# Optimization experiments

Measured on AMD Instinct MI355X. Metric: run time of the kernel, lower is better.

## Reference

```python
import jax, jax.numpy as jnp
import numpy as np

D_MODEL = 256
D_HID = 128
EPS = 1e-5
MASK_VALUE = -10000.0


def _layer_norm(x, scale, bias):
    mu = jnp.mean(x, axis=-1, keepdims=True)
    var = jnp.mean(jnp.square(x - mu), axis=-1, keepdims=True)
    return (x - mu) * jax.lax.rsqrt(var + EPS) * scale + bias


def setup_inputs() -> dict:
    key = jax.random.key(0)
    ks = jax.random.split(key, 8)
    B, S = 32, 1024
    std = 0.02
    return {
        "x": jax.random.normal(ks[0], (B, S, D_MODEL), dtype=jnp.float32),
        "ln1_scale": jnp.ones((D_MODEL,), jnp.float32),
        "ln1_bias": jnp.zeros((D_MODEL,), jnp.float32),
        "w_qkv": jax.random.normal(ks[1], (D_MODEL, 3 * D_MODEL), jnp.float32) * std,
        "b_qkv": jnp.zeros((3 * D_MODEL,), jnp.float32),
        "w_proj": jax.random.normal(ks[2], (D_MODEL, D_MODEL), jnp.float32) * std,
        "b_proj": jnp.zeros((D_MODEL,), jnp.float32),
        "ln2_scale": jnp.ones((D_MODEL,), jnp.float32),
        "ln2_bias": jnp.zeros((D_MODEL,), jnp.float32),
        "w_fc1": jax.random.normal(ks[3], (D_MODEL, D_HID), jnp.float32) * std,
        "b_fc1": jnp.zeros((D_HID,), jnp.float32),
        "w_fc2": jax.random.normal(ks[4], (D_HID, D_MODEL), jnp.float32) * std,
        "b_fc2": jnp.zeros((D_MODEL,), jnp.float32),
    }


def reference(x, ln1_scale, ln1_bias, w_qkv, b_qkv, w_proj, b_proj,
              ln2_scale, ln2_bias, w_fc1, b_fc1, w_fc2, b_fc2):
    B, S, D = x.shape
    # --- pre-LN self-attention ---
    residual = x
    h = _layer_norm(x, ln1_scale, ln1_bias)
    qkv = h @ w_qkv + b_qkv                       # [B, S, 3D]
    q, k, v = jnp.split(qkv, 3, axis=2)           # each [B, S, D]; 1 head, head_dim=D
    scale = 1.0 / jnp.sqrt(jnp.asarray(D, x.dtype))
    scores = jnp.einsum('bqd,bkd->bqk', q, k) * scale   # [B, S, S]
    causal = jnp.tril(jnp.ones((S, S), dtype=bool))
    scores = jnp.where(causal[None, :, :], scores, MASK_VALUE)
    attn = jax.nn.softmax(scores, axis=-1)        # dropout is identity (eval mode)
    out = jnp.einsum('bqk,bkd->bqd', attn, v)     # [B, S, D]
    out = out @ w_proj + b_proj
    x = out + residual
    # --- pre-LN MLP ---
    residual = x
    h = _layer_norm(x, ln2_scale, ln2_bias)
    h = jax.nn.relu(h @ w_fc1 + b_fc1)
    h = h @ w_fc2 + b_fc2
    return h + residual
```

## Files before the change

kernel.cpp:

```cpp
#include <hip/hip_runtime.h>
#include <hip/hip_bf16.h>

#define D_MODEL 256
#define D_HID   128
#define SEQ     1024
#define NBATCH  32
#define NROWS   (NBATCH * SEQ)
#define MASKV   -10000.0f
#define EPSLN   1e-5f

typedef unsigned short u16;
using bf16x8 = __attribute__((ext_vector_type(8))) short;
using f32x4  = __attribute__((ext_vector_type(4))) float;

union U8 { uint4 v; u16 s[8]; };

__device__ __forceinline__ float bf2f(u16 u) {
    unsigned int x = ((unsigned int)u) << 16;
    return __uint_as_float(x);
}
__device__ __forceinline__ u16 f2bf(float f) {
    unsigned int u = __float_as_uint(f);
    u += 0x7fff + ((u >> 16) & 1);
    return (u16)(u >> 16);
}
__device__ __forceinline__ void load4(const float* p, float* f) {
    float4 a = *(const float4*)p;
    f[0] = a.x; f[1] = a.y; f[2] = a.z; f[3] = a.w;
}
__device__ __forceinline__ void load4(const u16* p, float* f) {
    ushort4 v = *(const ushort4*)p;
    f[0] = bf2f(v.x); f[1] = bf2f(v.y); f[2] = bf2f(v.z); f[3] = bf2f(v.w);
}
__device__ __forceinline__ void gload16(const u16* g, u16* l) {
    __builtin_amdgcn_global_load_lds(
        (const __attribute__((address_space(1))) void*)g,
        (__attribute__((address_space(3))) void*)l, 16, 0, 0);
}

template <int CTRL>
__device__ __forceinline__ float dpp_mov(float v) {
    return __int_as_float(__builtin_amdgcn_update_dpp(
        0, __float_as_int(v), CTRL, 0xf, 0xf, true));
}
__device__ __forceinline__ float red16_max(float v) {
    v = fmaxf(v, dpp_mov<0xB1>(v));
    v = fmaxf(v, dpp_mov<0x4E>(v));
    v = fmaxf(v, dpp_mov<0x141>(v));
    v = fmaxf(v, dpp_mov<0x140>(v));
    return v;
}
__device__ __forceinline__ float red16_sum(float v) {
    v += dpp_mov<0xB1>(v);
    v += dpp_mov<0x4E>(v);
    v += dpp_mov<0x141>(v);
    v += dpp_mov<0x140>(v);
    return v;
}

__global__ __launch_bounds__(256) void transpose_weights(
    const float* __restrict__ wqkv, u16* __restrict__ wqkvT,
    const float* __restrict__ wproj, u16* __restrict__ wprojT,
    const float* __restrict__ wfc1, u16* __restrict__ wfc1T,
    const float* __restrict__ wfc2, u16* __restrict__ wfc2T) {
    int tid = blockIdx.x * 256 + threadIdx.x;
    int stride = gridDim.x * 256;
    for (int i = tid; i < 768 * 256; i += stride) {
        int n = i >> 8, k = i & 255;
        wqkvT[i] = f2bf(wqkv[k * 768 + n]);
    }
    for (int i = tid; i < 256 * 256; i += stride) {
        int n = i >> 8, k = i & 255;
        wprojT[i] = f2bf(wproj[k * 256 + n]);
    }
    for (int i = tid; i < 128 * 256; i += stride) {
        int n = i >> 8, k = i & 255;
        wfc1T[i] = f2bf(wfc1[k * 128 + n]);
    }
    for (int i = tid; i < 256 * 128; i += stride) {
        int n = i >> 7, k = i & 127;
        wfc2T[i] = f2bf(wfc2[k * 256 + n]);
    }
}

template <typename TX>
__global__ __launch_bounds__(256) void ln_fused(
    const TX* __restrict__ x, const float* __restrict__ gamma,
    const float* __restrict__ beta, u16* __restrict__ out) {
    int wave = threadIdx.x >> 6, lane = threadIdx.x & 63;
    int row = blockIdx.x * 4 + wave;
    float f[4];
    load4(x + (size_t)row * D_MODEL + lane * 4, f);
    float s  = f[0] + f[1] + f[2] + f[3];
    float sq = f[0] * f[0] + f[1] * f[1] + f[2] * f[2] + f[3] * f[3];
    #pragma unroll
    for (int off = 1; off < 64; off <<= 1) {
        s  += __shfl_xor(s, off);
        sq += __shfl_xor(sq, off);
    }
    float mu   = s * (1.0f / 256.0f);
    float var  = sq * (1.0f / 256.0f) - mu * mu;
    float rstd = rsqrtf(var + EPSLN);
    float g[4], be[4];
    load4(gamma + lane * 4, g);
    load4(beta + lane * 4, be);
    ushort4 o;
    o.x = f2bf((f[0] - mu) * rstd * g[0] + be[0]);
    o.y = f2bf((f[1] - mu) * rstd * g[1] + be[1]);
    o.z = f2bf((f[2] - mu) * rstd * g[2] + be[2]);
    o.w = f2bf((f[3] - mu) * rstd * g[3] + be[3]);
    *(ushort4*)(out + (size_t)row * D_MODEL + lane * 4) = o;
}

#define GT2_ELEMS (2 * 128 * 128)

template <int K>
__device__ __forceinline__ void gemm_tile2(
    const u16* __restrict__ A, const u16* __restrict__ BT,
    int m0, int n0, u16* lds, f32x4 acc[4][4]) {
    u16* ldsA = lds;
    u16* ldsB = lds + 128 * 128;
    const int tid = threadIdx.x;
    const int lane = tid & 63, wave = tid >> 6;
    const int wr = (wave >> 1) * 64, wc = (wave & 1) * 64;
    const int row = lane & 15, quad = lane >> 4;

    for (int ks = 0; ks < K; ks += 128) {
        __syncthreads();
        #pragma unroll
        for (int i = 0; i < 8; i++) {
            int blk = i * 4 + wave;
            int B = (blk << 10) + lane * 16;
            int r = B >> 8;
            int cb = (B & 255) ^ ((r & 7) << 4);
            gload16(A + (size_t)(m0 + r) * K + ks + (cb >> 1),
                    ldsA + (blk << 9));
            gload16(BT + (size_t)(n0 + r) * K + ks + (cb >> 1),
                    ldsB + (blk << 9));
        }
        __syncthreads();
        #pragma unroll
        for (int k0 = 0; k0 < 128; k0 += 32) {
            bf16x8 a[4], b[4];
            #pragma unroll
            for (int mi = 0; mi < 4; mi++) {
                int rr = wr + mi * 16 + row;
                a[mi] = *(const bf16x8*)(ldsA + rr * 128 +
                         ((k0 + quad * 8) ^ ((rr & 7) << 3)));
            }
            #pragma unroll
            for (int nj = 0; nj < 4; nj++) {
                int rr = wc + nj * 16 + row;
                b[nj] = *(const bf16x8*)(ldsB + rr * 128 +
                         ((k0 + quad * 8) ^ ((rr & 7) << 3)));
            }
            #pragma unroll
            for (int mi = 0; mi < 4; mi++)
                #pragma unroll
                for (int nj = 0; nj < 4; nj++)
                    acc[mi][nj] = __builtin_amdgcn_mfma_f32_16x16x32_bf16(
                        a[mi], b[nj], acc[mi][nj], 0, 0, 0);
        }
    }
}

#define ZERO_ACC4(acc)                                       \
    _Pragma("unroll") for (int i_ = 0; i_ < 4; i_++)         \
    _Pragma("unroll") for (int j_ = 0; j_ < 4; j_++)         \
    _Pragma("unroll") for (int e_ = 0; e_ < 4; e_++) acc[i_][j_][e_] = 0.0f;

#define EPILOG_IDX4                                          \
    int lane = threadIdx.x & 63, wave = threadIdx.x >> 6;    \
    int wr = (wave >> 1) * 64, wc = (wave & 1) * 64;         \
    int row = lane & 15, quad = lane >> 4;

__global__ __launch_bounds__(256) void gemm_qkv(
    const u16* __restrict__ h, const u16* __restrict__ wqkvT,
    const float* __restrict__ b_qkv,
    u16* __restrict__ q, u16* __restrict__ kk, u16* __restrict__ vT) {
    __shared__ u16 lds[GT2_ELEMS];
    f32x4 acc[4][4];
    ZERO_ACC4(acc)
    int m0 = blockIdx.x * 128, n0 = blockIdx.y * 128;
    gemm_tile2<256>(h, wqkvT, m0, n0, lds, acc);
    EPILOG_IDX4
    #pragma unroll
    for (int mi = 0; mi < 4; mi++) {
        #pragma unroll
        for (int nj = 0; nj < 4; nj++) {
            int gn = n0 + wc + nj * 16 + row;
            float bias = b_qkv[gn];
            int gm = m0 + wr + mi * 16 + quad * 4;
            if (gn < 256) {
                #pragma unroll
                for (int r = 0; r < 4; r++)
                    q[(size_t)(gm + r) * 256 + gn] =
                        f2bf((acc[mi][nj][r] + bias) * 0.0625f);
            } else if (gn < 512) {
                int col = gn - 256;
                #pragma unroll
                for (int r = 0; r < 4; r++)
                    kk[(size_t)(gm + r) * 256 + col] = f2bf(acc[mi][nj][r] + bias);
            } else {
                int d = gn - 512;
                int b = gm >> 10, s = gm & 1023;
                ushort4 pack;
                pack.x = f2bf(acc[mi][nj][0] + bias);
                pack.y = f2bf(acc[mi][nj][1] + bias);
                pack.z = f2bf(acc[mi][nj][2] + bias);
                pack.w = f2bf(acc[mi][nj][3] + bias);
                *(ushort4*)(vT + ((size_t)(b * 256 + d) << 10) + s) = pack;
            }
        }
    }
}

__global__ __launch_bounds__(256) void gemm_proj(
    const u16* __restrict__ ao, const u16* __restrict__ wprojT,
    const float* __restrict__ b_proj, const float* __restrict__ x_in,
    u16* __restrict__ x2) {
    __shared__ u16 lds[GT2_ELEMS];
    f32x4 acc[4][4];
    ZERO_ACC4(acc)
    int m0 = blockIdx.x * 128, n0 = blockIdx.y * 128;
    gemm_tile2<256>(ao, wprojT, m0, n0, lds, acc);
    EPILOG_IDX4
    #pragma unroll
    for (int mi = 0; mi < 4; mi++)
        #pragma unroll
        for (int nj = 0; nj < 4; nj++) {
            int gn = n0 + wc + nj * 16 + row;
            float bias = b_proj[gn];
            int gm = m0 + wr + mi * 16 + quad * 4;
            #pragma unroll
            for (int r = 0; r < 4; r++) {
                size_t idx = (size_t)(gm + r) * 256 + gn;
                x2[idx] = f2bf(acc[mi][nj][r] + bias + x_in[idx]);
            }
        }
}

__global__ __launch_bounds__(256) void gemm_mlp(
    const u16* __restrict__ x2, const float* __restrict__ g2,
    const float* __restrict__ be2,
    const u16* __restrict__ wfc1T, const float* __restrict__ b_fc1,
    const u16* __restrict__ wfc2T, const float* __restrict__ b_fc2,
    float* __restrict__ out) {
    __shared__ u16 lds[65536];
    u16* ldsB1 = lds + 32768;
    u16* ldsA1 = lds + 49152;
    const int tid = threadIdx.x;
    const int lane = tid & 63, wave = tid >> 6;
    const int rowl = lane & 15, quad = lane >> 4;
    const int wr = (wave >> 1) * 64, wc = (wave & 1) * 64;
    const int m0 = blockIdx.x * 128;

    #pragma unroll
    for (int i = 0; i < 16; i++) {
        int blk = i * 4 + wave;
        int B = (blk << 10) + lane * 16;
        int r = B >> 9;
        int cb = (B & 511) ^ ((r & 7) << 4);
        gload16(x2 + (size_t)(m0 + r) * 256 + (cb >> 1), lds + (B >> 1));
    }
    #pragma unroll
    for (int i = 0; i < 8; i++) {
        int blk = i * 4 + wave;
        int B = (blk << 10) + lane * 16;
        int r = B >> 8;
        int cb = (B & 255) ^ ((r & 7) << 4);
        gload16(wfc1T + (size_t)r * 256 + 0 + (cb >> 1), ldsB1 + (B >> 1));
    }
    __syncthreads();

    {
        float4 g4  = *(const float4*)(g2 + lane * 4);
        float4 be4 = *(const float4*)(be2 + lane * 4);
        #pragma unroll 4
        for (int i = 0; i < 32; i++) {
            int r = wave + i * 4;
            char* p = (char*)lds + r * 512 + ((lane * 8) ^ ((r & 7) << 4));
            ushort4 v = *(ushort4*)p;
            float f0 = bf2f(v.x), f1 = bf2f(v.y), f2v = bf2f(v.z), f3 = bf2f(v.w);
            float s  = f0 + f1 + f2v + f3;
            float sq = f0*f0 + f1*f1 + f2v*f2v + f3*f3;
            s = red16_sum(s);   s += __shfl_xor(s, 16);   s += __shfl_xor(s, 32);
            sq = red16_sum(sq); sq += __shfl_xor(sq, 16); sq += __shfl_xor(sq, 32);
            float mu   = s * (1.0f / 256.0f);
            float var  = sq * (1.0f / 256.0f) - mu * mu;
            float rstd = rsqrtf(var + EPSLN);
            ushort4 o;
            o.x = f2bf((f0  - mu) * rstd * g4.x + be4.x);
            o.y = f2bf((f1  - mu) * rstd * g4.y + be4.y);
            o.z = f2bf((f2v - mu) * rstd * g4.z + be4.z);
            o.w = f2bf((f3  - mu) * rstd * g4.w + be4.w);
            *(ushort4*)p = o;
        }
    }
    __syncthreads();

    f32x4 acc1[4][4];
    ZERO_ACC4(acc1)
    #pragma unroll
    for (int ks = 0; ks < 256; ks += 128) {
        if (ks) {
            __syncthreads();
            #pragma unroll
            for (int i = 0; i < 8; i++) {
                int blk = i * 4 + wave;
                int B = (blk << 10) + lane * 16;
                int r = B >> 8;
                int cb = (B & 255) ^ ((r & 7) << 4);
                gload16(wfc1T + (size_t)r * 256 + ks + (cb >> 1),
                        ldsB1 + (B >> 1));
            }
            __syncthreads();
        }
        #pragma unroll
        for (int k0 = 0; k0 < 128; k0 += 32) {
            bf16x8 a[4], b[4];
            #pragma unroll
            for (int mi = 0; mi < 4; mi++) {
                int rr = wr + mi * 16 + rowl;
                a[mi] = *(const bf16x8*)((const char*)lds + rr * 512 +
                         ((((ks + k0 + quad * 8) << 1)) ^ ((rr & 7) << 4)));
            }
            #pragma unroll
            for (int nj = 0; nj < 4; nj++) {
                int rb = wc + nj * 16 + rowl;
                b[nj] = *(const bf16x8*)((const char*)ldsB1 + rb * 256 +
                         ((((k0 + quad * 8) << 1)) ^ ((rb & 7) << 4)));
            }
            #pragma unroll
            for (int mi = 0; mi < 4; mi++)
                #pragma unroll
                for (int nj = 0; nj < 4; nj++)
                    acc1[mi][nj] = __builtin_amdgcn_mfma_f32_16x16x32_bf16(
                        a[mi], b[nj], acc1[mi][nj], 0, 0, 0);
        }
    }
    #pragma unroll
    for (int mi = 0; mi < 4; mi++)
        #pragma unroll
        for (int nj = 0; nj < 4; nj++) {
            int gn_l = wc + nj * 16 + rowl;
            float bias = b_fc1[gn_l];
            #pragma unroll
            for (int r = 0; r < 4; r++) {
                int gm_l = wr + mi * 16 + quad * 4 + r;
                *(u16*)((char*)ldsA1 + gm_l * 256 +
                        (((gn_l << 1)) ^ ((gm_l & 7) << 4))) =
                    f2bf(fmaxf(acc1[mi][nj][r] + bias, 0.0f));
            }
        }
    __syncthreads();

    #pragma unroll
    for (int i = 0; i < 16; i++) {
        int blk = i * 4 + wave;
        int B = (blk << 10) + lane * 16;
        int r = B >> 8;
        int cb = (B & 255) ^ ((r & 7) << 4);
        gload16(wfc2T + (size_t)r * 128 + (cb >> 1), lds + (B >> 1));
    }
    __syncthreads();

    const int wc2 = (wave & 1) * 128;
    f32x4 acc2[4][8];
    #pragma unroll
    for (int mi = 0; mi < 4; mi++)
        #pragma unroll
        for (int nj = 0; nj < 8; nj++)
            #pragma unroll
            for (int e = 0; e < 4; e++) acc2[mi][nj][e] = 0.0f;
    #pragma unroll
    for (int k0 = 0; k0 < 128; k0 += 32) {
        bf16x8 a[4], b[8];
        #pragma unroll
        for (int mi = 0; mi < 4; mi++) {
            int rr = wr + mi * 16 + rowl;
            a[mi] = *(const bf16x8*)((const char*)ldsA1 + rr * 256 +
                     ((((k0 + quad * 8) << 1)) ^ ((rr & 7) << 4)));
        }
        #pragma unroll
        for (int nj = 0; nj < 8; nj++) {
            int rb = wc2 + nj * 16 + rowl;
            b[nj] = *(const bf16x8*)((const char*)lds + rb * 256 +
                     ((((k0 + quad * 8) << 1)) ^ ((rb & 7) << 4)));
        }
        #pragma unroll
        for (int mi = 0; mi < 4; mi++)
            #pragma unroll
            for (int nj = 0; nj < 8; nj++)
                acc2[mi][nj] = __builtin_amdgcn_mfma_f32_16x16x32_bf16(
                    a[mi], b[nj], acc2[mi][nj], 0, 0, 0);
    }
    #pragma unroll
    for (int mi = 0; mi < 4; mi++)
        #pragma unroll
        for (int nj = 0; nj < 8; nj++) {
            int gn = wc2 + nj * 16 + rowl;
            float bias = b_fc2[gn];
            int gm = m0 + wr + mi * 16 + quad * 4;
            #pragma unroll
            for (int r = 0; r < 4; r++) {
                size_t idx = (size_t)(gm + r) * 256 + gn;
                out[idx] = acc2[mi][nj][r] + bias + bf2f(x2[idx]);
            }
        }
}

__constant__ unsigned char WQT[24] = {7,15,15,14,14,6,13,13,
                                      4,10,10,5,11,11,12,12,
                                      9,0,1,2,3,9,8,8};
__constant__ unsigned char WH[24]  = {2,0,1,0,1,2,0,1,
                                      2,0,1,2,0,1,0,1,
                                      0,2,2,2,2,1,0,1};

__global__ __launch_bounds__(256) void attn_kernel(
    const u16* __restrict__ q, const u16* __restrict__ k,
    const u16* __restrict__ vT, u16* __restrict__ ao,
    u16* __restrict__ part, float* __restrict__ ml) {
    __shared__ u16 k_lds[2][32 * 256];
    __shared__ u16 v_lds[256 * 32];
    __shared__ u16 p_lds[4][16 * 40];

    int j = blockIdx.x;
    int b = j & 31, w = j >> 5;
    int qt = WQT[w], hh = WH[w];
    int lo, hi;
    if (hh == 2) { lo = 0; hi = 2 * qt + 2; }
    else         { lo = hh * (qt + 1); hi = lo + qt + 1; }

    int tid = threadIdx.x;
    int lane = tid & 63, wave = tid >> 6;
    int row = lane & 15, quad = lane >> 4;
    int q0 = qt * 64;
    int qrow0 = q0 + wave * 16;

    const u16* qb = q + ((size_t)b << 10) * 256;
    const u16* kb = k + ((size_t)b << 10) * 256;
    const u16* vb = vT + (((size_t)b * 256) << 10);

    const int kxor = (row & 7) << 3;
    const int vxor = (row & 6) << 2;

    bf16x8 qf[8];
    #pragma unroll
    for (int kf = 0; kf < 8; kf++)
        qf[kf] = *(const bf16x8*)(qb + (size_t)(qrow0 + row) * 256 + kf * 32 + quad * 8);

    f32x4 o[16];
    #pragma unroll
    for (int n = 0; n < 16; n++)
        #pragma unroll
        for (int e = 0; e < 4; e++) o[n][e] = 0.0f;
    float m_i[4], l_i[4];
    #pragma unroll
    for (int r = 0; r < 4; r++) { m_i[r] = -1e30f; l_i[r] = 0.0f; }

    int wlast = 2 * qt + (wave >> 1);

    auto stageK = [&](int bf, int kt) {
        int k0 = kt << 5;
        #pragma unroll
        for (int c = 0; c < 4; c++) {
            int blk = wave * 4 + c;
            int B = (blk << 10) + lane * 16;
            int rk = B >> 9;
            int ck = (B & 511) ^ ((rk & 7) << 4);
            gload16(kb + (size_t)(k0 + rk) * 256 + (ck >> 1),
                    &k_lds[bf][blk << 9]);
        }
    };
    auto stageV = [&](int kt) {
        int k0 = kt << 5;
        #pragma unroll
        for (int c = 0; c < 4; c++) {
            int blk = wave * 4 + c;
            int B = (blk << 10) + lane * 16;
            int rv = B >> 6;
            int cv = (B & 63) ^ ((rv & 6) << 3);
            gload16(vb + ((size_t)rv << 10) + k0 + (cv >> 1),
                    &v_lds[blk << 9]);
        }
    };

    stageK(0, lo);
    stageV(lo);
    __syncthreads();

    for (int kt = lo; kt < hi; kt++) {
        int cur = (kt - lo) & 1;
        if (kt + 1 < hi) stageK(cur ^ 1, kt + 1);
        if (kt <= wlast) {
            const u16* kl = k_lds[cur];
            const u16* vl = v_lds;

            f32x4 sf[2];
            #pragma unroll
            for (int jn = 0; jn < 2; jn++)
                #pragma unroll
                for (int e = 0; e < 4; e++) sf[jn][e] = 0.0f;
            __builtin_amdgcn_s_setprio(1);
            #pragma unroll
            for (int kf = 0; kf < 8; kf++)
                #pragma unroll
                for (int jn = 0; jn < 2; jn++) {
                    bf16x8 bfrag = *(const bf16x8*)(kl +
                        ((((jn * 16 + row) * 256) + kf * 32 + quad * 8) ^ kxor));
                    sf[jn] = __builtin_amdgcn_mfma_f32_16x16x32_bf16(
                        qf[kf], bfrag, sf[jn], 0, 0, 0);
                }
            __builtin_amdgcn_s_setprio(0);

            int kk0 = kt * 32;
            bool diag = (kt == wlast);
            int qrow = qrow0 + quad * 4;
            float sv[2][4];
            #pragma unroll
            for (int jn = 0; jn < 2; jn++)
                #pragma unroll
                for (int r = 0; r < 4; r++) {
                    float v = sf[jn][r];
                    if (diag && (kk0 + jn * 16 + row > qrow + r)) v = MASKV;
                    sv[jn][r] = v;
                }

            float pmax[4];
            int need = 0;
            #pragma unroll
            for (int r = 0; r < 4; r++) {
                pmax[r] = red16_max(fmaxf(sv[0][r], sv[1][r]));
                need |= (pmax[r] > m_i[r] + 8.0f) ? 1 : 0;
            }
            if (__any(need)) {
                #pragma unroll
                for (int r = 0; r < 4; r++) {
                    float mnew = fmaxf(m_i[r], pmax[r]);
                    float al = __expf(m_i[r] - mnew);
                    m_i[r] = mnew;
                    l_i[r] *= al;
                    #pragma unroll
                    for (int n = 0; n < 16; n++) o[n][r] *= al;
                }
            }
            #pragma unroll
            for (int r = 0; r < 4; r++) {
                float ps = 0.0f;
                #pragma unroll
                for (int jn = 0; jn < 2; jn++) {
                    sv[jn][r] = __expf(sv[jn][r] - m_i[r]);
                    ps += sv[jn][r];
                }
                l_i[r] += red16_sum(ps);
            }

            u16* pw = p_lds[wave];
            #pragma unroll
            for (int jn = 0; jn < 2; jn++)
                #pragma unroll
                for (int r = 0; r < 4; r++)
                    pw[(quad * 4 + r) * 40 + jn * 16 + row] = f2bf(sv[jn][r]);
            bf16x8 pf = *(const bf16x8*)(pw + row * 40 + quad * 8);

            __builtin_amdgcn_s_setprio(1);
            #pragma unroll
            for (int n = 0; n < 16; n++) {
                bf16x8 bv = *(const bf16x8*)(vl +
                    ((((n * 16 + row) * 32) + quad * 8) ^ vxor));
                o[n] = __builtin_amdgcn_mfma_f32_16x16x32_bf16(pf, bv, o[n], 0, 0, 0);
            }
            __builtin_amdgcn_s_setprio(0);
        }
        __syncthreads();
        if (kt + 1 < hi) stageV(kt + 1);
        __syncthreads();
    }

    if (hh == 2) {
        float inv[4];
        #pragma unroll
        for (int r = 0; r < 4; r++) inv[r] = 1.0f / l_i[r];
        u16* aob = ao + (((size_t)b << 10) + qrow0) * 256;
        #pragma unroll
        for (int r = 0; r < 4; r++)
            #pragma unroll
            for (int n = 0; n < 16; n++)
                aob[(size_t)(quad * 4 + r) * 256 + n * 16 + row] =
                    f2bf(o[n][r] * inv[r]);
    } else {
        int p = (((b << 3) | (qt - 8)) << 1) | hh;
        u16* pb = part + (((size_t)p) << 6) * 256;
        #pragma unroll
        for (int r = 0; r < 4; r++) {
            int rt = wave * 16 + quad * 4 + r;
            #pragma unroll
            for (int n = 0; n < 16; n++)
                pb[(size_t)rt * 256 + n * 16 + row] = f2bf(o[n][r]);
        }
        if (row == 0) {
            #pragma unroll
            for (int r = 0; r < 4; r++) {
                int rt = wave * 16 + quad * 4 + r;
                float2 v2; v2.x = m_i[r]; v2.y = l_i[r];
                *(float2*)(ml + ((size_t)((p << 6) + rt)) * 2) = v2;
            }
        }
    }
}

__global__ __launch_bounds__(256) void attn_merge(
    const u16* __restrict__ part, const float* __restrict__ ml,
    u16* __restrict__ ao) {
    int j = blockIdx.x;
    int b = j >> 3, qi = j & 7;
    int t = threadIdx.x;
    int r = t >> 2, cq = t & 3;
    int pA = j << 1, pB = pA | 1;
    const float* mlA = ml + ((size_t)(pA << 6) + r) * 2;
    const float* mlB = ml + ((size_t)(pB << 6) + r) * 2;
    float mA = mlA[0], lA = mlA[1];
    float mB = mlB[0], lB = mlB[1];
    float m  = fmaxf(mA, mB);
    float eA = __expf(mA - m), eB = __expf(mB - m);
    float inv = 1.0f / (lA * eA + lB * eB);
    float sA = eA * inv, sB = eB * inv;
    const u16* oA = part + (((size_t)(pA << 6) + r) * 256) + cq * 64;
    const u16* oB = part + (((size_t)(pB << 6) + r) * 256) + cq * 64;
    u16* dst = ao + ((size_t)((b << 10) + 512 + (qi << 6) + r)) * 256 + cq * 64;
    #pragma unroll
    for (int u = 0; u < 8; u++) {
        U8 a, bb, o;
        a.v  = *(const uint4*)(oA + u * 8);
        bb.v = *(const uint4*)(oB + u * 8);
        #pragma unroll
        for (int e = 0; e < 8; e++)
            o.s[e] = f2bf(bf2f(a.s[e]) * sA + bf2f(bb.s[e]) * sB);
        *(uint4*)(dst + u * 8) = o.v;
    }
}

extern "C" void kernel_launch(void* const* d_in, const int* in_sizes, int n_in,
                              void* d_out, int out_size, void* d_ws, size_t ws_size,
                              hipStream_t stream) {
    const float* x      = (const float*)d_in[0];
    const float* ln1_s  = (const float*)d_in[1];
    const float* ln1_b  = (const float*)d_in[2];
    const float* w_qkv  = (const float*)d_in[3];
    const float* b_qkv  = (const float*)d_in[4];
    const float* w_proj = (const float*)d_in[5];
    const float* b_proj = (const float*)d_in[6];
    const float* ln2_s  = (const float*)d_in[7];
    const float* ln2_b  = (const float*)d_in[8];
    const float* w_fc1  = (const float*)d_in[9];
    const float* b_fc1  = (const float*)d_in[10];
    const float* w_fc2  = (const float*)d_in[11];
    const float* b_fc2  = (const float*)d_in[12];
    float* out = (float*)d_out;

    u16* h  = (u16*)d_out;
    u16* h2 = h + (size_t)NROWS * 256;

    u16* W = (u16*)d_ws;
    u16* wqkvT  = W;
    u16* wprojT = wqkvT + 196608;
    u16* wfc1T  = wprojT + 65536;
    u16* wfc2T  = wfc1T + 32768;
    u16* buf1   = wfc2T + 32768;
    u16* buf2   = buf1 + (size_t)NROWS * 256;
    u16* buf3   = buf2 + (size_t)NROWS * 256;

    u16*   part  = h;
    float* mlbuf = (float*)h2;

    transpose_weights<<<dim3(64), dim3(256), 0, stream>>>(
        w_qkv, wqkvT, w_proj, wprojT, w_fc1, wfc1T, w_fc2, wfc2T);
    ln_fused<float><<<dim3(NROWS / 4), dim3(256), 0, stream>>>(
        x, ln1_s, ln1_b, h);
    gemm_qkv<<<dim3(NROWS / 128, 6), dim3(256), 0, stream>>>(
        h, wqkvT, b_qkv, buf1, buf2, buf3);
    attn_kernel<<<dim3(768), dim3(256), 0, stream>>>(
        buf1, buf2, buf3, buf1, part, mlbuf);
    attn_merge<<<dim3(256), dim3(256), 0, stream>>>(
        part, mlbuf, buf1);
    gemm_proj<<<dim3(NROWS / 128, 2), dim3(256), 0, stream>>>(
        buf1, wprojT, b_proj, x, buf2);
    gemm_mlp<<<dim3(NROWS / 128), dim3(256), 0, stream>>>(
        buf2, ln2_s, ln2_b, wfc1T, b_fc1, wfc2T, b_fc2, out);
}
```

Before: 250.8 us.

## Load K/V fragments directly from global memory in attention, dropping LDS staging

The attention kernel no longer stages K and V tiles through shared memory with double buffering and block-wide barriers. Each wave now reads its MFMA operand fragments straight from global memory and iterates only up to its own causal limit, with no __syncthreads. Launch bounds request 4 blocks per CU to raise occupancy now that LDS use is small. The risk is that each wave re-fetches K and V from L2 or HBM with no LDS reuse across the four waves, and global load latency sits directly in front of the MFMAs.

```diff
diff --git a/kernel.cpp b/kernel.cpp
--- a/kernel.cpp
+++ b/kernel.cpp
@@ -417,12 +417,10 @@
                                       2,0,1,2,0,1,0,1,
                                       0,2,2,2,2,1,0,1};
 
-__global__ __launch_bounds__(256) void attn_kernel(
+__global__ __launch_bounds__(256, 4) void attn_kernel(
     const u16* __restrict__ q, const u16* __restrict__ k,
     const u16* __restrict__ vT, u16* __restrict__ ao,
     u16* __restrict__ part, float* __restrict__ ml) {
-    __shared__ u16 k_lds[2][32 * 256];
-    __shared__ u16 v_lds[256 * 32];
     __shared__ u16 p_lds[4][16 * 40];
 
     int j = blockIdx.x;
@@ -442,9 +440,6 @@
     const u16* kb = k + ((size_t)b << 10) * 256;
     const u16* vb = vT + (((size_t)b * 256) << 10);
 
-    const int kxor = (row & 7) << 3;
-    const int vxor = (row & 6) << 2;
-
     bf16x8 qf[8];
     #pragma unroll
     for (int kf = 0; kf < 8; kf++)
@@ -460,122 +455,87 @@
     for (int r = 0; r < 4; r++) { m_i[r] = -1e30f; l_i[r] = 0.0f; }
 
     int wlast = 2 * qt + (wave >> 1);
-
-    auto stageK = [&](int bf, int kt) {
-        int k0 = kt << 5;
-        #pragma unroll
-        for (int c = 0; c < 4; c++) {
-            int blk = wave * 4 + c;
-            int B = (blk << 10) + lane * 16;
-            int rk = B >> 9;
-            int ck = (B & 511) ^ ((rk & 7) << 4);
-            gload16(kb + (size_t)(k0 + rk) * 256 + (ck >> 1),
-                    &k_lds[bf][blk << 9]);
-        }
-    };
-    auto stageV = [&](int kt) {
-        int k0 = kt << 5;
-        #pragma unroll
-        for (int c = 0; c < 4; c++) {
-            int blk = wave * 4 + c;
-            int B = (blk << 10) + lane * 16;
-            int rv = B >> 6;
-            int cv = (B & 63) ^ ((rv & 6) << 3);
-            gload16(vb + ((size_t)rv << 10) + k0 + (cv >> 1),
-                    &v_lds[blk << 9]);
-        }
-    };
-
-    stageK(0, lo);
-    stageV(lo);
-    __syncthreads();
-
-    for (int kt = lo; kt < hi; kt++) {
-        int cur = (kt - lo) & 1;
-        if (kt + 1 < hi) stageK(cur ^ 1, kt + 1);
-        if (kt <= wlast) {
-            const u16* kl = k_lds[cur];
-            const u16* vl = v_lds;
-
-            f32x4 sf[2];
-            #pragma unroll
-            for (int jn = 0; jn < 2; jn++)
+    int myhi = min(hi, wlast + 1);
+
+    const u16* kfrag = kb + (size_t)row * 256 + quad * 8;
+    const u16* vfrag = vb + (size_t)row * 1024 + quad * 8;
+
+    for (int kt = lo; kt < myhi; kt++) {
+        const u16* kbase = kfrag + (size_t)(kt * 32) * 256;
+        f32x4 sf[2];
+        #pragma unroll
+        for (int jn = 0; jn < 2; jn++)
+            #pragma unroll
+            for (int e = 0; e < 4; e++) sf[jn][e] = 0.0f;
+        __builtin_amdgcn_s_setprio(1);
+        #pragma unroll
+        for (int kf = 0; kf < 8; kf++)
+            #pragma unroll
+            for (int jn = 0; jn < 2; jn++) {
+                bf16x8 bfrag = *(const bf16x8*)(kbase + (size_t)(jn * 16) * 256 + kf * 32);
+                sf[jn] = __builtin_amdgcn_mfma_f32_16x16x32_bf16(
+                    qf[kf], bfrag, sf[jn], 0, 0, 0);
+            }
+        __builtin_amdgcn_s_setprio(0);
+
+        int kk0 = kt * 32;
+        bool diag = (kt == wlast);
+        int qrow = qrow0 + quad * 4;
+        float sv[2][4];
+        #pragma unroll
+        for (int jn = 0; jn < 2; jn++)
+            #pragma unroll
+            for (int r = 0; r < 4; r++) {
+                float v = sf[jn][r];
+                if (diag && (kk0 + jn * 16 + row > qrow + r)) v = MASKV;
+                sv[jn][r] = v;
+            }
+
+        float pmax[4];
+        int need = 0;
+        #pragma unroll
+        for (int r = 0; r < 4; r++) {
+            pmax[r] = red16_max(fmaxf(sv[0][r], sv[1][r]));
+            need |= (pmax[r] > m_i[r] + 8.0f) ? 1 : 0;
+        }
+        if (__any(need)) {
+            #pragma unroll
+            for (int r = 0; r < 4; r++) {
+                float mnew = fmaxf(m_i[r], pmax[r]);
+                float al = __expf(m_i[r] - mnew);
+                m_i[r] = mnew;
+                l_i[r] *= al;
                 #pragma unroll
-                for (int e = 0; e < 4; e++) sf[jn][e] = 0.0f;
-            __builtin_amdgcn_s_setprio(1);
-            #pragma unroll
-            for (int kf = 0; kf < 8; kf++)
-                #pragma unroll
-                for (int jn = 0; jn < 2; jn++) {
-                    bf16x8 bfrag = *(const bf16x8*)(kl +
-                        ((((jn * 16 + row) * 256) + kf * 32 + quad * 8) ^ kxor));
-                    sf[jn] = __builtin_amdgcn_mfma_f32_16x16x32_bf16(
-                        qf[kf], bfrag, sf[jn], 0, 0, 0);
-                }
-            __builtin_amdgcn_s_setprio(0);
-
-            int kk0 = kt * 32;
-            bool diag = (kt == wlast);
-            int qrow = qrow0 + quad * 4;
-            float sv[2][4];
-            #pragma unroll
-            for (int jn = 0; jn < 2; jn++)
-                #pragma unroll
-                for (int r = 0; r < 4; r++) {
-                    float v = sf[jn][r];
-                    if (diag && (kk0 + jn * 16 + row > qrow + r)) v = MASKV;
-                    sv[jn][r] = v;
-                }
-
-            float pmax[4];
-            int need = 0;
-            #pragma unroll
-            for (int r = 0; r < 4; r++) {
-                pmax[r] = red16_max(fmaxf(sv[0][r], sv[1][r]));
-                need |= (pmax[r] > m_i[r] + 8.0f) ? 1 : 0;
-            }
-            if (__any(need)) {
-                #pragma unroll
-                for (int r = 0; r < 4; r++) {
-                    float mnew = fmaxf(m_i[r], pmax[r]);
-                    float al = __expf(m_i[r] - mnew);
-                    m_i[r] = mnew;
-                    l_i[r] *= al;
-                    #pragma unroll
-                    for (int n = 0; n < 16; n++) o[n][r] *= al;
-                }
-            }
-            #pragma unroll
-            for (int r = 0; r < 4; r++) {
-                float ps = 0.0f;
-                #pragma unroll
-                for (int jn = 0; jn < 2; jn++) {
-                    sv[jn][r] = __expf(sv[jn][r] - m_i[r]);
-                    ps += sv[jn][r];
-                }
-                l_i[r] += red16_sum(ps);
-            }
-
-            u16* pw = p_lds[wave];
-            #pragma unroll
-            for (int jn = 0; jn < 2; jn++)
-                #pragma unroll
-                for (int r = 0; r < 4; r++)
-                    pw[(quad * 4 + r) * 40 + jn * 16 + row] = f2bf(sv[jn][r]);
-            bf16x8 pf = *(const bf16x8*)(pw + row * 40 + quad * 8);
-
-            __builtin_amdgcn_s_setprio(1);
-            #pragma unroll
-            for (int n = 0; n < 16; n++) {
-                bf16x8 bv = *(const bf16x8*)(vl +
-                    ((((n * 16 + row) * 32) + quad * 8) ^ vxor));
-                o[n] = __builtin_amdgcn_mfma_f32_16x16x32_bf16(pf, bv, o[n], 0, 0, 0);
-            }
-            __builtin_amdgcn_s_setprio(0);
-        }
-        __syncthreads();
-        if (kt + 1 < hi) stageV(kt + 1);
-        __syncthreads();
+                for (int n = 0; n < 16; n++) o[n][r] *= al;
+            }
+        }
+        #pragma unroll
+        for (int r = 0; r < 4; r++) {
+            float ps = 0.0f;
+            #pragma unroll
+            for (int jn = 0; jn < 2; jn++) {
+                sv[jn][r] = __expf(sv[jn][r] - m_i[r]);
+                ps += sv[jn][r];
+            }
+            l_i[r] += red16_sum(ps);
+        }
+
+        u16* pw = p_lds[wave];
+        #pragma unroll
+        for (int jn = 0; jn < 2; jn++)
+            #pragma unroll
+            for (int r = 0; r < 4; r++)
+                pw[(quad * 4 + r) * 40 + jn * 16 + row] = f2bf(sv[jn][r]);
+        bf16x8 pf = *(const bf16x8*)(pw + row * 40 + quad * 8);
+
+        const u16* vbase = vfrag + kt * 32;
+        __builtin_amdgcn_s_setprio(1);
+        #pragma unroll
+        for (int n = 0; n < 16; n++) {
+            bf16x8 bv = *(const bf16x8*)(vbase + (size_t)(n * 16) * 1024);
+            o[n] = __builtin_amdgcn_mfma_f32_16x16x32_bf16(pf, bv, o[n], 0, 0, 0);
+        }
+        __builtin_amdgcn_s_setprio(0);
     }
 
     if (hh == 2) {
```

After: 340.3 us. 1.36x slower.

## Double-buffer V tiles in attention and reorder block work schedule

Applied to the files above, without the earlier changes.

V is now double-buffered in LDS like K, so the next tile's K and V are both prefetched at the top of each iteration. This removes one __syncthreads and the serialized V load that previously sat after compute. The block-to-tile mapping tables are also reordered so heavier tiles launch first and lighter ones last. LDS usage rises by 16 KB per block, which may reduce occupancy.

```diff
diff --git a/kernel.cpp b/kernel.cpp
--- a/kernel.cpp
+++ b/kernel.cpp
@@ -410,19 +410,17 @@
         }
 }
 
-__constant__ unsigned char WQT[24] = {7,15,15,14,14,6,13,13,
-                                      4,10,10,5,11,11,12,12,
-                                      9,0,1,2,3,9,8,8};
-__constant__ unsigned char WH[24]  = {2,0,1,0,1,2,0,1,
-                                      2,0,1,2,0,1,0,1,
-                                      0,2,2,2,2,1,0,1};
+__constant__ unsigned char WQT[24] = {7,15,15,14,14,6,13,13,12,12,5,11,
+                                      11,10,10,4,9,9,8,8,3,2,1,0};
+__constant__ unsigned char WH[24]  = {2,0,1,0,1,2,0,1,0,1,2,0,
+                                      1,0,1,2,0,1,0,1,2,2,2,2};
 
 __global__ __launch_bounds__(256) void attn_kernel(
     const u16* __restrict__ q, const u16* __restrict__ k,
     const u16* __restrict__ vT, u16* __restrict__ ao,
     u16* __restrict__ part, float* __restrict__ ml) {
     __shared__ u16 k_lds[2][32 * 256];
-    __shared__ u16 v_lds[256 * 32];
+    __shared__ u16 v_lds[2][256 * 32];
     __shared__ u16 p_lds[4][16 * 40];
 
     int j = blockIdx.x;
@@ -461,7 +459,7 @@
 
     int wlast = 2 * qt + (wave >> 1);
 
-    auto stageK = [&](int bf, int kt) {
+    auto stage = [&](int bf, int kt) {
         int k0 = kt << 5;
         #pragma unroll
         for (int c = 0; c < 4; c++) {
@@ -471,31 +469,22 @@
             int ck = (B & 511) ^ ((rk & 7) << 4);
             gload16(kb + (size_t)(k0 + rk) * 256 + (ck >> 1),
                     &k_lds[bf][blk << 9]);
-        }
-    };
-    auto stageV = [&](int kt) {
-        int k0 = kt << 5;
-        #pragma unroll
-        for (int c = 0; c < 4; c++) {
-            int blk = wave * 4 + c;
-            int B = (blk << 10) + lane * 16;
             int rv = B >> 6;
             int cv = (B & 63) ^ ((rv & 6) << 3);
             gload16(vb + ((size_t)rv << 10) + k0 + (cv >> 1),
-                    &v_lds[blk << 9]);
+                    &v_lds[bf][blk << 9]);
         }
     };
 
-    stageK(0, lo);
-    stageV(lo);
+    stage(0, lo);
     __syncthreads();
 
     for (int kt = lo; kt < hi; kt++) {
         int cur = (kt - lo) & 1;
-        if (kt + 1 < hi) stageK(cur ^ 1, kt + 1);
+        if (kt + 1 < hi) stage(cur ^ 1, kt + 1);
         if (kt <= wlast) {
             const u16* kl = k_lds[cur];
-            const u16* vl = v_lds;
+            const u16* vl = v_lds[cur];
 
             f32x4 sf[2];
             #pragma unroll
@@ -573,8 +562,6 @@
             }
             __builtin_amdgcn_s_setprio(0);
         }
-        __syncthreads();
-        if (kt + 1 < hi) stageV(kt + 1);
         __syncthreads();
     }
 
```

After: 246.4 us. Within noise of the previous version (-1.8%).
